# Kernel tuning notes

Measured on AMD Instinct MI355X. Metric: run time of the kernel, lower is better.

The kernel has to match this reference:

```python
import jax, jax.numpy as jnp
import numpy as np

B, C, D, H, W = 2, 128, 16, 16, 16
DSIM = PSIM = GDIM = 64
N_ROUNDS = 3  # pool_strides = [1, 1, 1]


def build_neighbors(D, H, W):
    """Cross-graph neighbors: for node (i,j,k), all nodes sharing an axis line,
    self kept exactly once (dedup). Returns sorted [N, D+H+W-2] int indices."""
    N = D * H * W
    i, j, k = np.unravel_index(np.arange(N), (D, H, W))
    ax0 = np.arange(D)[None, :] * (H * W) + (j * W + k)[:, None]          # [N, D] (contains self)
    ax1 = (i * H * W)[:, None] + np.arange(H)[None, :] * W + k[:, None]   # [N, H]
    ax2 = (i * H * W + j * W)[:, None] + np.arange(W)[None, :]            # [N, W]
    self_idx = np.arange(N)
    ax1 = ax1[ax1 != self_idx[:, None]].reshape(N, H - 1)
    ax2 = ax2[ax2 != self_idx[:, None]].reshape(N, W - 1)
    return np.sort(np.concatenate([ax0, ax1, ax2], axis=1), axis=1)       # [N, D+H+W-2]


def l2norm(x, axis):
    return x / (1e-6 + jnp.linalg.norm(x, axis=axis, keepdims=True))


def setup_inputs() -> dict:
    key = jax.random.key(0)
    ks = jax.random.split(key, 13)
    s = 0.05
    return {
        "x": jax.random.normal(ks[0], (B, C, D, H, W), jnp.float32),
        "G_w": jax.random.normal(ks[1], (GDIM, C), jnp.float32) * s,
        "G_b": jax.random.normal(ks[2], (GDIM,), jnp.float32) * s,
        "theta_w": jax.random.normal(ks[3], (DSIM, C), jnp.float32) * s,
        "theta_b": jax.random.normal(ks[4], (DSIM,), jnp.float32) * s,
        "phi_w": jax.random.normal(ks[5], (DSIM, C), jnp.float32) * s,
        "phi_b": jax.random.normal(ks[6], (DSIM,), jnp.float32) * s,
        "r_w": jax.random.normal(ks[7], (C, GDIM), jnp.float32) * s,
        "r_b": jax.random.normal(ks[8], (C,), jnp.float32) * s,
        "geo_theta_w": jax.random.normal(ks[9], (PSIM, 3), jnp.float32) * s,
        "geo_theta_b": jax.random.normal(ks[10], (PSIM,), jnp.float32) * s,
        "geo_phi_w": jax.random.normal(ks[11], (PSIM, 3), jnp.float32) * s,
        "geo_phi_b": jax.random.normal(ks[12], (PSIM,), jnp.float32) * s,
    }


def reference(x, G_w, G_b, theta_w, theta_b, phi_w, phi_b, r_w, r_b,
              geo_theta_w, geo_theta_b, geo_phi_w, geo_phi_b):
    Bx, Cx, Dx, Hx, Wx = x.shape
    N = Dx * Hx * Wx
    nbr = jnp.asarray(build_neighbors(Dx, Hx, Wx))                         # [N, E]
    # geo positional features: normalized grid coords in [-0.5, 0.5], batch-identical
    coords = jnp.stack(jnp.meshgrid(jnp.arange(Dx), jnp.arange(Hx), jnp.arange(Wx),
                                    indexing='ij'), axis=-1).reshape(N, 3).astype(x.dtype)
    p = coords / (jnp.asarray([Dx, Hx, Wx], x.dtype) - 1.0) - 0.5          # [N, 3]
    p_theta = p @ geo_theta_w.T + geo_theta_b                              # [N, PSIM]
    p_phi = p @ geo_phi_w.T + geo_phi_b                                    # [N, PSIM]
    f_p = jnp.einsum('np,nep->ne', p_theta, p_phi[nbr])                    # [N, E]
    f_p = l2norm(f_p, axis=0)                                              # do_norm: l2 over node dim
    f_p = jax.nn.relu(f_p)[None]                                           # [1, N, E]

    h = x.reshape(Bx, Cx, N).transpose(0, 2, 1)                            # [B, N, C]
    for _ in range(N_ROUNDS):
        x_theta = h @ theta_w.T + theta_b                                  # [B, N, DSIM]
        x_phi_e = (h @ phi_w.T + phi_b)[:, nbr]                            # [B, N, E, DSIM]
        f = jnp.einsum('bnd,bned->bne', x_theta, x_phi_e)                  # [B, N, E]
        f = l2norm(f, axis=1)                                              # do_norm over node dim
        attn = jax.nn.softmax(f + f_p, axis=-1)                            # merge 'softmax'
        x_g_e = (h @ G_w.T + G_b)[:, nbr]                                  # [B, N, E, GDIM]
        y = jnp.einsum('bne,bneg->bng', attn, x_g_e)                       # [B, N, GDIM]
        h = h + (y @ r_w.T + r_b)                                          # residual (group_norm=False)
    return h.transpose(0, 2, 1).reshape(Bx, Cx, Dx, Hx, Wx)
```

## Files before the change

### kernel.cpp

```cpp
#include <hip/hip_runtime.h>
#include <math.h>

#define BB 2
#define CC 128
#define NN 4096
#define EE 46
#define FS 48
#define DS 64
#define CPAD 16
#define NSH 16

__global__ __launch_bounds__(256) void k_setup(
    const float* __restrict__ x,
    int* __restrict__ nbr,
    float* __restrict__ colnorm_p, float* __restrict__ colnorm_f,
    float* __restrict__ h)
{
    __shared__ float xs[32 * 65];
    const int t = threadIdx.x, bid = blockIdx.x;
    const int gtid = bid * 256 + t;

    if (gtid < EE * NSH * CPAD) colnorm_p[gtid] = 0.f;
    if (gtid < 3 * BB * EE * NSH * CPAD) colnorm_f[gtid] = 0.f;

    if (gtid < NN) {
        int n = gtid;
        int i = n >> 8, j = (n >> 4) & 15, k = n & 15;
        int ia = 0, ib = 0, ic = 0;
        for (int e = 0; e < EE; ++e) {
            int va = (ia < 16) ? ia * 256 + j * 16 + k : 0x7fffffff;
            int jb = ib + (ib >= j ? 1 : 0);
            int vb = (ib < 15) ? i * 256 + jb * 16 + k : 0x7fffffff;
            int kc = ic + (ic >= k ? 1 : 0);
            int vc = (ic < 15) ? i * 256 + j * 16 + kc : 0x7fffffff;
            int v;
            if (va < vb && va < vc)      { v = va; ++ia; }
            else if (vb < vc)            { v = vb; ++ib; }
            else                         { v = vc; ++ic; }
            nbr[n * EE + e] = v;
        }
    }
    {
        int n0 = (bid & 63) * 64, c0 = ((bid >> 6) & 3) * 32, b = bid >> 8;
        for (int q = t; q < 2048; q += 256) {
            int cl = q >> 6, nl = q & 63;
            xs[cl * 65 + nl] = x[(size_t)(b * CC + c0 + cl) * NN + n0 + nl];
        }
        __syncthreads();
        for (int q = t; q < 2048; q += 256) {
            int nl = q >> 5, cl = q & 31;
            h[(size_t)(b * NN + n0 + nl) * CC + c0 + cl] = xs[cl * 65 + nl];
        }
    }
}

__global__ __launch_bounds__(256) void k_proj(
    const float* __restrict__ h,
    const float* __restrict__ th_w, const float* __restrict__ th_b,
    const float* __restrict__ ph_w, const float* __restrict__ ph_b,
    const float* __restrict__ G_w,  const float* __restrict__ G_b,
    float* __restrict__ T, float* __restrict__ P, float* __restrict__ Gx)
{
    __shared__ __align__(16) float smf[12288];
    const int t = threadIdx.x;
    const int row0 = (blockIdx.x & 255) * 32;
    const int cgp = blockIdx.x >> 8;
    const float* w    = cgp == 0 ? th_w : cgp == 1 ? ph_w : G_w;
    const float* bias = cgp == 0 ? th_b : cgp == 1 ? ph_b : G_b;
    float* o          = cgp == 0 ? T    : cgp == 1 ? P    : Gx;
    float4* hs4 = (float4*)smf;
    float4* ws4 = (float4*)smf + 1024;
    const float4* h4 = (const float4*)h;
    const float4* w4 = (const float4*)w;
    for (int q = t; q < 1024; q += 256) {
        int row = q >> 5, kc = q & 31;
        hs4[row * 32 + (kc ^ row)] = h4[(size_t)(row0 + row) * 32 + kc];
    }
    for (int q = t; q < 2048; q += 256) {
        int row = q >> 5, kc = q & 31;
        ws4[row * 32 + (kc ^ (row & 31))] = w4[q];
    }
    __syncthreads();
    const int rt = t >> 4, m = t & 15;
    float acc[2][4] = {{0, 0, 0, 0}, {0, 0, 0, 0}};
    for (int kc = 0; kc < 32; ++kc) {
        float4 a0 = hs4[(2 * rt) * 32 + (kc ^ (2 * rt))];
        float4 a1 = hs4[(2 * rt + 1) * 32 + (kc ^ (2 * rt + 1))];
        float4 wv[4];
#pragma unroll
        for (int i = 0; i < 4; ++i) {
            int c = m + 16 * i;
            wv[i] = ws4[c * 32 + (kc ^ (c & 31))];
        }
#pragma unroll
        for (int i = 0; i < 4; ++i) {
            acc[0][i] += a0.x * wv[i].x + a0.y * wv[i].y
                       + a0.z * wv[i].z + a0.w * wv[i].w;
            acc[1][i] += a1.x * wv[i].x + a1.y * wv[i].y
                       + a1.z * wv[i].z + a1.w * wv[i].w;
        }
    }
#pragma unroll
    for (int i = 0; i < 4; ++i) {
        float bv = bias[m + 16 * i];
#pragma unroll
        for (int rr = 0; rr < 2; ++rr)
            o[(size_t)(row0 + 2 * rt + rr) * DS + m + 16 * i] = acc[rr][i] + bv;
    }
}

__device__ __forceinline__ int axis_node(int axis, int line, int s) {
    if (axis == 0) return s * 256 + line;
    if (axis == 1) return (line >> 4) * 256 + s * 16 + (line & 15);
    return line * 16 + s;
}

__global__ __launch_bounds__(256) void k_fax(
    const float* __restrict__ T, const float* __restrict__ P,
    const float* __restrict__ gt_w, const float* __restrict__ gt_b,
    const float* __restrict__ gp_w, const float* __restrict__ gp_b,
    float* __restrict__ f, float* __restrict__ colnorm_f,
    float* __restrict__ f_p, float* __restrict__ colnorm_p)
{
    __shared__ __align__(16) float4 Ts4[272];
    __shared__ __align__(16) float4 Ps4[272];
    __shared__ float sq[64];

    const int t = threadIdx.x;
    const int line = blockIdx.x, axis = blockIdx.y;
    const bool geo = (blockIdx.z == BB);
    const int b = geo ? 0 : blockIdx.z;
    float* dst = geo ? f_p : f;
    float* cn  = geo ? colnorm_p : colnorm_f;

    {
        int s = t >> 4, kc = t & 15;
        int nrow = axis_node(axis, line, s);
        if (!geo) {
            Ts4[s * 17 + kc] = ((const float4*)T)[((size_t)b * NN + nrow) * 16 + kc];
            Ps4[s * 17 + kc] = ((const float4*)P)[((size_t)b * NN + nrow) * 16 + kc];
        } else {
            int i = nrow >> 8, j = (nrow >> 4) & 15, k = nrow & 15;
            float p0 = i * (1.f / 15.f) - 0.5f;
            float p1 = j * (1.f / 15.f) - 0.5f;
            float p2 = k * (1.f / 15.f) - 0.5f;
            float tv[4], pv[4];
#pragma unroll
            for (int d = 0; d < 4; ++d) {
                int dim = kc * 4 + d;
                tv[d] = p0 * gt_w[dim * 3] + p1 * gt_w[dim * 3 + 1]
                      + p2 * gt_w[dim * 3 + 2] + gt_b[dim];
                pv[d] = p0 * gp_w[dim * 3] + p1 * gp_w[dim * 3 + 1]
                      + p2 * gp_w[dim * 3 + 2] + gp_b[dim];
            }
            Ts4[s * 17 + kc] = make_float4(tv[0], tv[1], tv[2], tv[3]);
            Ps4[s * 17 + kc] = make_float4(pv[0], pv[1], pv[2], pv[3]);
        }
    }
    if (t < 64) sq[t] = 0.f;
    __syncthreads();

    const int node = t >> 4, slot = t & 15;
    const int n = axis_node(axis, line, node);
    const int m = axis_node(axis, line, slot);
    const int jj = (n >> 4) & 15, kk = n & 15;
    bool valid = !((axis == 1 && slot == jj) || (axis == 2 && slot == kk));

    float dot = 0.f;
#pragma unroll
    for (int kc = 0; kc < 16; ++kc) {
        float4 a = Ts4[node * 17 + kc];
        float4 p = Ps4[slot * 17 + kc];
        dot += a.x * p.x + a.y * p.y + a.z * p.z + a.w * p.w;
    }

    if (valid) {
        dst[((size_t)b * NN + n) * FS + axis * 16 + slot] = dot;
        const int jk = n & 255, base = n & ~255;
        int d = m - jk;
        int cD = d <= 0 ? 0 : min(16, (d + 255) >> 8);
        int hd = m - base - kk;
        int cHr = hd <= 0 ? 0 : min(16, (hd + 15) >> 4);
        int cH = cHr - (jj < cHr ? 1 : 0);
        int wd = m - (n - kk);
        int cWr = wd <= 0 ? 0 : min(16, wd);
        int cW = cWr - (kk < cWr ? 1 : 0);
        int e = cD + cH + cW;
        atomicAdd(&sq[e], dot * dot);
    }
    __syncthreads();
    if (t < EE)
        atomicAdd(cn + ((size_t)(b * EE + t) * NSH + (line & (NSH - 1))) * CPAD,
                  sq[t]);
}

__global__ __launch_bounds__(256) void k_agg(
    const int* __restrict__ nbr,
    const float* __restrict__ f, const float* __restrict__ f_p,
    const float* __restrict__ colnorm_p, const float* __restrict__ colnorm_f,
    const float* __restrict__ Gx, float* __restrict__ y)
{
    __shared__ __align__(16) float Gl[16 * 64];
    __shared__ float wmat[256];
    __shared__ float nf[64], np[64];

    const int t = threadIdx.x;
    const int line = blockIdx.x, axis = blockIdx.y, b = blockIdx.z;

    if (t < EE) {
        float sf = 0.f, sp = 0.f;
#pragma unroll
        for (int s = 0; s < NSH; ++s) {
            sf += colnorm_f[((size_t)(b * EE + t) * NSH + s) * CPAD];
            sp += colnorm_p[((size_t)t * NSH + s) * CPAD];
        }
        nf[t] = 1.f / (1e-6f + sqrtf(sf));
        np[t] = 1.f / (1e-6f + sqrtf(sp));
    }
    wmat[t] = 0.f;
    {
        int s = t >> 4, c4 = t & 15;
        int nrow = axis_node(axis, line, s);
        ((float4*)Gl)[s * 16 + c4] =
            ((const float4*)Gx)[((size_t)b * NN + nrow) * 16 + c4];
    }
    __syncthreads();

    const int wv = t >> 6, l = t & 63;
    for (int ii = 0; ii < 4; ++ii) {
        int sn = wv * 4 + ii;
        int n = axis_node(axis, line, sn);
        float fvv = -INFINITY; int ax = 0, slot = 0;
        if (l < EE) {
            int m = nbr[n * EE + l];
            int x = m ^ n;
            if (x == 0)       { ax = 0; slot = n >> 8; }
            else if (x < 16)  { ax = 2; slot = m & 15; }
            else if (x < 256) { ax = 1; slot = (m >> 4) & 15; }
            else              { ax = 0; slot = m >> 8; }
            int col = ax * 16 + slot;
            float fpv = f_p[(size_t)n * FS + col] * np[l];
            fpv = fpv > 0.f ? fpv : 0.f;
            fvv = f[(size_t)(b * NN + n) * FS + col] * nf[l] + fpv;
        }
        float mx = fvv;
        for (int o = 32; o; o >>= 1) mx = fmaxf(mx, __shfl_down(mx, o));
        mx = __shfl(mx, 0);
        float ex = (l < EE) ? expf(fvv - mx) : 0.f;
        float sm = ex;
        for (int o = 32; o; o >>= 1) sm += __shfl_down(sm, o);
        sm = __shfl(sm, 0);
        if (l < EE && ax == axis) wmat[sn * 16 + slot] = ex / sm;
    }
    __syncthreads();

    float acc[4] = {0.f, 0.f, 0.f, 0.f};
    for (int s = 0; s < 16; ++s) {
        float gv = Gl[s * 64 + l];
        acc[0] += wmat[(wv * 4 + 0) * 16 + s] * gv;
        acc[1] += wmat[(wv * 4 + 1) * 16 + s] * gv;
        acc[2] += wmat[(wv * 4 + 2) * 16 + s] * gv;
        acc[3] += wmat[(wv * 4 + 3) * 16 + s] * gv;
    }
    float* ya = y + ((size_t)axis * BB + b) * NN * DS;
#pragma unroll
    for (int kk = 0; kk < 4; ++kk) {
        int n = axis_node(axis, line, wv * 4 + kk);
        ya[(size_t)n * DS + l] = acc[kk];
    }
}

template <int LAST>
__global__ __launch_bounds__(256) void k_epi(
    const float* __restrict__ y, const float* __restrict__ r_w,
    const float* __restrict__ r_b,
    float* __restrict__ h, float* __restrict__ out)
{
    __shared__ __align__(16) float smf[6528];
    float4* ys4  = (float4*)smf;
    float4* rws4 = (float4*)smf + 544;
    float*  dls  = smf;

    const int t = threadIdx.x;
    const int rt0 = blockIdx.x * 32;
    const int c0 = blockIdx.y * 64;
    const float4* y4  = (const float4*)y;
    const float4* rw4 = (const float4*)r_w;
    for (int q = t; q < 512; q += 256) {
        int row = q >> 4, kc = q & 15;
        float4 a = y4[(size_t)(rt0 + row) * 16 + kc];
        float4 bb = y4[((size_t)BB * NN + rt0 + row) * 16 + kc];
        float4 c = y4[((size_t)2 * BB * NN + rt0 + row) * 16 + kc];
        float4 s;
        s.x = a.x + bb.x + c.x; s.y = a.y + bb.y + c.y;
        s.z = a.z + bb.z + c.z; s.w = a.w + bb.w + c.w;
        ys4[row * 17 + kc] = s;
    }
    for (int q = t; q < 1024; q += 256) {
        int row = q >> 4, kc = q & 15;
        rws4[row * 17 + kc] = rw4[(size_t)(c0 + row) * 16 + kc];
    }
    __syncthreads();

    const int rt = t >> 4, m = t & 15;
    float acc[2][4] = {{0, 0, 0, 0}, {0, 0, 0, 0}};
    for (int kc = 0; kc < 16; ++kc) {
        float4 a0 = ys4[(2 * rt) * 17 + kc];
        float4 a1 = ys4[(2 * rt + 1) * 17 + kc];
        float4 wv[4];
#pragma unroll
        for (int i = 0; i < 4; ++i)
            wv[i] = rws4[(m + 16 * i) * 17 + kc];
#pragma unroll
        for (int i = 0; i < 4; ++i) {
            acc[0][i] += a0.x * wv[i].x + a0.y * wv[i].y
                       + a0.z * wv[i].z + a0.w * wv[i].w;
            acc[1][i] += a1.x * wv[i].x + a1.y * wv[i].y
                       + a1.z * wv[i].z + a1.w * wv[i].w;
        }
    }

    if (!LAST) {
#pragma unroll
        for (int rr = 0; rr < 2; ++rr) {
            size_t r = (size_t)rt0 + 2 * rt + rr;
#pragma unroll
            for (int i = 0; i < 4; ++i) {
                int c = c0 + m + 16 * i;
                h[r * CC + c] += acc[rr][i] + r_b[c];
            }
        }
    } else {
        float res[2][4];
#pragma unroll
        for (int rr = 0; rr < 2; ++rr) {
            size_t r = (size_t)rt0 + 2 * rt + rr;
#pragma unroll
            for (int i = 0; i < 4; ++i) {
                int c = c0 + m + 16 * i;
                res[rr][i] = h[r * CC + c] + acc[rr][i] + r_b[c];
            }
        }
        __syncthreads();
#pragma unroll
        for (int rr = 0; rr < 2; ++rr)
#pragma unroll
            for (int i = 0; i < 4; ++i)
                dls[(2 * rt + rr) * 68 + m + 16 * i] = res[rr][i];
        __syncthreads();
        const int b = rt0 >> 12, n0g = rt0 & (NN - 1);
        for (int q = t; q < 2048; q += 256) {
            int cl = q >> 5, nl = q & 31;
            out[(size_t)(b * CC + c0 + cl) * NN + n0g + nl] = dls[nl * 68 + cl];
        }
    }
}

extern "C" void kernel_launch(void* const* d_in, const int* in_sizes, int n_in,
                              void* d_out, int out_size, void* d_ws, size_t ws_size,
                              hipStream_t stream) {
    const float* x    = (const float*)d_in[0];
    const float* G_w  = (const float*)d_in[1];
    const float* G_b  = (const float*)d_in[2];
    const float* th_w = (const float*)d_in[3];
    const float* th_b = (const float*)d_in[4];
    const float* ph_w = (const float*)d_in[5];
    const float* ph_b = (const float*)d_in[6];
    const float* r_w  = (const float*)d_in[7];
    const float* r_b  = (const float*)d_in[8];
    const float* gt_w = (const float*)d_in[9];
    const float* gt_b = (const float*)d_in[10];
    const float* gp_w = (const float*)d_in[11];
    const float* gp_b = (const float*)d_in[12];
    float* out = (float*)d_out;

    char* ws = (char*)d_ws;
    size_t off = 0;
    auto alloc = [&](size_t bytes) {
        char* p = ws + off;
        off = (off + bytes + 255) & ~size_t(255);
        return p;
    };
    int*   nbr       = (int*)  alloc((size_t)NN * EE * sizeof(int));
    float* f_p       = (float*)alloc((size_t)NN * FS * sizeof(float));
    float* colnorm_p = (float*)alloc((size_t)EE * NSH * CPAD * sizeof(float));
    float* colnorm_f = (float*)alloc((size_t)3 * BB * EE * NSH * CPAD * sizeof(float));
    float* h         = (float*)alloc((size_t)BB * NN * CC * sizeof(float));
    float* T         = (float*)alloc((size_t)BB * NN * DS * sizeof(float));
    float* P         = (float*)alloc((size_t)BB * NN * DS * sizeof(float));
    float* Gx        = (float*)alloc((size_t)BB * NN * DS * sizeof(float));
    float* f         = (float*)alloc((size_t)BB * NN * FS * sizeof(float));
    float* y         = (float*)alloc((size_t)3 * BB * NN * DS * sizeof(float));
    (void)ws_size; (void)in_sizes; (void)n_in; (void)out_size;

    k_setup<<<512, 256, 0, stream>>>(x, nbr, colnorm_p, colnorm_f, h);
    for (int r = 0; r < 3; ++r) {
        float* cn = colnorm_f + (size_t)r * BB * EE * NSH * CPAD;
        k_proj<<<768, 256, 0, stream>>>(h, th_w, th_b, ph_w, ph_b, G_w, G_b,
                                        T, P, Gx);
        int zext = (r == 0) ? BB + 1 : BB;
        k_fax<<<dim3(256, 3, zext), 256, 0, stream>>>(T, P, gt_w, gt_b,
                                                      gp_w, gp_b, f, cn,
                                                      f_p, colnorm_p);
        k_agg<<<dim3(256, 3, BB), 256, 0, stream>>>(nbr, f, f_p, colnorm_p, cn,
                                                    Gx, y);
        if (r < 2)
            k_epi<0><<<dim3(256, 2), 256, 0, stream>>>(y, r_w, r_b, h, out);
        else
            k_epi<1><<<dim3(256, 2), 256, 0, stream>>>(y, r_w, r_b, h, out);
    }
}
```

Measured before the change: 165.7 us.

## Fuse residual epilogue into next round's projection kernel with ping-pong h buffers

The residual update h += y·r_wᵀ + r_b from rounds one and two now runs inside the following k_proj launch, so the separate epilogue kernels and one round trip of h through global memory are gone. Every k_proj block (three channel groups per row tile) recomputes the same 32x128 residual GEMM tile redundantly, and only group 0 writes the updated h to a second buffer, giving a ping-pong scheme. This removes two launches and an h read-modify-write, but it triples the epilogue arithmetic and the y reads, and it adds an r_w staging step before the projection weights are loaded.

```diff
diff --git a/kernel.cpp b/kernel.cpp
--- a/kernel.cpp
+++ b/kernel.cpp
@@ -54,8 +54,11 @@
     }
 }
 
+template <int EPI>
 __global__ __launch_bounds__(256) void k_proj(
-    const float* __restrict__ h,
+    const float* __restrict__ hin, float* __restrict__ hout,
+    const float* __restrict__ y,
+    const float* __restrict__ r_w, const float* __restrict__ r_b,
     const float* __restrict__ th_w, const float* __restrict__ th_b,
     const float* __restrict__ ph_w, const float* __restrict__ ph_b,
     const float* __restrict__ G_w,  const float* __restrict__ G_b,
@@ -70,17 +73,74 @@
     float* o          = cgp == 0 ? T    : cgp == 1 ? P    : Gx;
     float4* hs4 = (float4*)smf;
     float4* ws4 = (float4*)smf + 1024;
-    const float4* h4 = (const float4*)h;
+    const float4* h4 = (const float4*)hin;
     const float4* w4 = (const float4*)w;
+
     for (int q = t; q < 1024; q += 256) {
         int row = q >> 5, kc = q & 31;
         hs4[row * 32 + (kc ^ row)] = h4[(size_t)(row0 + row) * 32 + kc];
     }
-    for (int q = t; q < 2048; q += 256) {
-        int row = q >> 5, kc = q & 31;
-        ws4[row * 32 + (kc ^ (row & 31))] = w4[q];
-    }
-    __syncthreads();
+    if (EPI) {
+        const float4* rw4 = (const float4*)r_w;
+        for (int i2 = t; i2 < 2048; i2 += 256) {
+            int c = i2 >> 4, g4 = i2 & 15;
+            ws4[c * 16 + ((g4 + c) & 15)] = rw4[i2];
+        }
+        __syncthreads();
+        const int rt = t >> 4, m = t & 15;
+        const float4* y4 = (const float4*)y;
+        float acc[2][8] = {};
+        for (int g4 = 0; g4 < 16; ++g4) {
+            size_t ra = (size_t)(row0 + 2 * rt) * 16 + g4;
+            size_t rb2 = ra + 16;
+            float4 a0 = y4[ra], a1 = y4[(size_t)BB * NN * 16 + ra],
+                   a2 = y4[(size_t)2 * BB * NN * 16 + ra];
+            float4 b0 = y4[rb2], b1 = y4[(size_t)BB * NN * 16 + rb2],
+                   b2 = y4[(size_t)2 * BB * NN * 16 + rb2];
+            float4 ya, yb;
+            ya.x = a0.x + a1.x + a2.x; ya.y = a0.y + a1.y + a2.y;
+            ya.z = a0.z + a1.z + a2.z; ya.w = a0.w + a1.w + a2.w;
+            yb.x = b0.x + b1.x + b2.x; yb.y = b0.y + b1.y + b2.y;
+            yb.z = b0.z + b1.z + b2.z; yb.w = b0.w + b1.w + b2.w;
+#pragma unroll
+            for (int i = 0; i < 8; ++i) {
+                int c = m + 16 * i;
+                float4 wv = ws4[c * 16 + ((g4 + c) & 15)];
+                acc[0][i] += ya.x * wv.x + ya.y * wv.y + ya.z * wv.z + ya.w * wv.w;
+                acc[1][i] += yb.x * wv.x + yb.y * wv.y + yb.z * wv.z + yb.w * wv.w;
+            }
+        }
+        float* hsf = smf;
+#pragma unroll
+        for (int rr = 0; rr < 2; ++rr) {
+            int row = 2 * rt + rr;
+#pragma unroll
+            for (int i = 0; i < 8; ++i) {
+                int c = m + 16 * i;
+                int f4idx = row * 32 + ((c >> 2) ^ row);
+                hsf[f4idx * 4 + (c & 3)] += acc[rr][i] + r_b[c];
+            }
+        }
+        __syncthreads();
+        if (cgp == 0) {
+            float4* ho4 = (float4*)hout;
+            for (int q = t; q < 1024; q += 256) {
+                int row = q >> 5, kc = q & 31;
+                ho4[(size_t)(row0 + row) * 32 + kc] = hs4[row * 32 + (kc ^ row)];
+            }
+        }
+        for (int q = t; q < 2048; q += 256) {
+            int row = q >> 5, kc = q & 31;
+            ws4[row * 32 + (kc ^ (row & 31))] = w4[q];
+        }
+    } else {
+        for (int q = t; q < 2048; q += 256) {
+            int row = q >> 5, kc = q & 31;
+            ws4[row * 32 + (kc ^ (row & 31))] = w4[q];
+        }
+    }
+    __syncthreads();
+
     const int rt = t >> 4, m = t & 15;
     float acc[2][4] = {{0, 0, 0, 0}, {0, 0, 0, 0}};
     for (int kc = 0; kc < 32; ++kc) {
@@ -270,11 +330,10 @@
     }
 }
 
-template <int LAST>
-__global__ __launch_bounds__(256) void k_epi(
+__global__ __launch_bounds__(256) void k_epi_last(
     const float* __restrict__ y, const float* __restrict__ r_w,
     const float* __restrict__ r_b,
-    float* __restrict__ h, float* __restrict__ out)
+    const float* __restrict__ h, float* __restrict__ out)
 {
     __shared__ __align__(16) float smf[6528];
     float4* ys4  = (float4*)smf;
@@ -320,39 +379,27 @@
         }
     }
 
-    if (!LAST) {
-#pragma unroll
-        for (int rr = 0; rr < 2; ++rr) {
-            size_t r = (size_t)rt0 + 2 * rt + rr;
-#pragma unroll
-            for (int i = 0; i < 4; ++i) {
-                int c = c0 + m + 16 * i;
-                h[r * CC + c] += acc[rr][i] + r_b[c];
-            }
-        }
-    } else {
-        float res[2][4];
-#pragma unroll
-        for (int rr = 0; rr < 2; ++rr) {
-            size_t r = (size_t)rt0 + 2 * rt + rr;
-#pragma unroll
-            for (int i = 0; i < 4; ++i) {
-                int c = c0 + m + 16 * i;
-                res[rr][i] = h[r * CC + c] + acc[rr][i] + r_b[c];
-            }
-        }
-        __syncthreads();
-#pragma unroll
-        for (int rr = 0; rr < 2; ++rr)
-#pragma unroll
-            for (int i = 0; i < 4; ++i)
-                dls[(2 * rt + rr) * 68 + m + 16 * i] = res[rr][i];
-        __syncthreads();
-        const int b = rt0 >> 12, n0g = rt0 & (NN - 1);
-        for (int q = t; q < 2048; q += 256) {
-            int cl = q >> 5, nl = q & 31;
-            out[(size_t)(b * CC + c0 + cl) * NN + n0g + nl] = dls[nl * 68 + cl];
-        }
+    float res[2][4];
+#pragma unroll
+    for (int rr = 0; rr < 2; ++rr) {
+        size_t r = (size_t)rt0 + 2 * rt + rr;
+#pragma unroll
+        for (int i = 0; i < 4; ++i) {
+            int c = c0 + m + 16 * i;
+            res[rr][i] = h[r * CC + c] + acc[rr][i] + r_b[c];
+        }
+    }
+    __syncthreads();
+#pragma unroll
+    for (int rr = 0; rr < 2; ++rr)
+#pragma unroll
+        for (int i = 0; i < 4; ++i)
+            dls[(2 * rt + rr) * 68 + m + 16 * i] = res[rr][i];
+    __syncthreads();
+    const int b = rt0 >> 12, n0g = rt0 & (NN - 1);
+    for (int q = t; q < 2048; q += 256) {
+        int cl = q >> 5, nl = q & 31;
+        out[(size_t)(b * CC + c0 + cl) * NN + n0g + nl] = dls[nl * 68 + cl];
     }
 }
 
@@ -385,7 +432,8 @@
     float* f_p       = (float*)alloc((size_t)NN * FS * sizeof(float));
     float* colnorm_p = (float*)alloc((size_t)EE * NSH * CPAD * sizeof(float));
     float* colnorm_f = (float*)alloc((size_t)3 * BB * EE * NSH * CPAD * sizeof(float));
-    float* h         = (float*)alloc((size_t)BB * NN * CC * sizeof(float));
+    float* hA        = (float*)alloc((size_t)BB * NN * CC * sizeof(float));
+    float* hB        = (float*)alloc((size_t)BB * NN * CC * sizeof(float));
     float* T         = (float*)alloc((size_t)BB * NN * DS * sizeof(float));
     float* P         = (float*)alloc((size_t)BB * NN * DS * sizeof(float));
     float* Gx        = (float*)alloc((size_t)BB * NN * DS * sizeof(float));
@@ -393,20 +441,40 @@
     float* y         = (float*)alloc((size_t)3 * BB * NN * DS * sizeof(float));
     (void)ws_size; (void)in_sizes; (void)n_in; (void)out_size;
 
-    k_setup<<<512, 256, 0, stream>>>(x, nbr, colnorm_p, colnorm_f, h);
-    for (int r = 0; r < 3; ++r) {
-        float* cn = colnorm_f + (size_t)r * BB * EE * NSH * CPAD;
-        k_proj<<<768, 256, 0, stream>>>(h, th_w, th_b, ph_w, ph_b, G_w, G_b,
-                                        T, P, Gx);
-        int zext = (r == 0) ? BB + 1 : BB;
-        k_fax<<<dim3(256, 3, zext), 256, 0, stream>>>(T, P, gt_w, gt_b,
-                                                      gp_w, gp_b, f, cn,
-                                                      f_p, colnorm_p);
+    k_setup<<<512, 256, 0, stream>>>(x, nbr, colnorm_p, colnorm_f, hA);
+
+    k_proj<0><<<768, 256, 0, stream>>>(hA, nullptr, nullptr, r_w, r_b,
+                                       th_w, th_b, ph_w, ph_b, G_w, G_b,
+                                       T, P, Gx);
+    k_fax<<<dim3(256, 3, BB + 1), 256, 0, stream>>>(T, P, gt_w, gt_b,
+                                                    gp_w, gp_b, f, colnorm_f,
+                                                    f_p, colnorm_p);
+    k_agg<<<dim3(256, 3, BB), 256, 0, stream>>>(nbr, f, f_p, colnorm_p,
+                                                colnorm_f, Gx, y);
+
+    {
+        float* cn = colnorm_f + (size_t)1 * BB * EE * NSH * CPAD;
+        k_proj<1><<<768, 256, 0, stream>>>(hA, hB, y, r_w, r_b,
+                                           th_w, th_b, ph_w, ph_b, G_w, G_b,
+                                           T, P, Gx);
+        k_fax<<<dim3(256, 3, BB), 256, 0, stream>>>(T, P, gt_w, gt_b,
+                                                    gp_w, gp_b, f, cn,
+                                                    f_p, colnorm_p);
         k_agg<<<dim3(256, 3, BB), 256, 0, stream>>>(nbr, f, f_p, colnorm_p, cn,
                                                     Gx, y);
-        if (r < 2)
-            k_epi<0><<<dim3(256, 2), 256, 0, stream>>>(y, r_w, r_b, h, out);
-        else
-            k_epi<1><<<dim3(256, 2), 256, 0, stream>>>(y, r_w, r_b, h, out);
-    }
-}
+    }
+
+    {
+        float* cn = colnorm_f + (size_t)2 * BB * EE * NSH * CPAD;
+        k_proj<1><<<768, 256, 0, stream>>>(hB, hA, y, r_w, r_b,
+                                           th_w, th_b, ph_w, ph_b, G_w, G_b,
+                                           T, P, Gx);
+        k_fax<<<dim3(256, 3, BB), 256, 0, stream>>>(T, P, gt_w, gt_b,
+                                                    gp_w, gp_b, f, cn,
+                                                    f_p, colnorm_p);
+        k_agg<<<dim3(256, 3, BB), 256, 0, stream>>>(nbr, f, f_p, colnorm_p, cn,
+                                                    Gx, y);
+    }
+
+    k_epi_last<<<dim3(256, 2), 256, 0, stream>>>(y, r_w, r_b, hA, out);
+}
```

Measured after the change: 174.0 us. 5.0% more time.
